# Kernel optimization log

Measured on AMD Instinct MI355X. Metric: run time of the kernel, lower is better.

## Reference

```python
import jax, jax.numpy as jnp
import numpy as np

# ---- fan-beam geometry config (uniform path: no pmatrix, uniform SID/SDD/angle/offcenter) ----
SID = 750.0          # source-to-isocenter distance (mm)
SDD = 1250.0         # source-to-detector distance (mm)
VIEWS = 128          # number of projection angles
NDET = 512           # detector element count
DET_ELT = 1.2        # detector element size (mm)
DET_OFF = 0.0        # detector offcenter (mm)
START_ANGLE = 0.0    # degrees
TOTAL_ANGLE = 360.0  # degrees
IMG_DIM = 256        # image is IMG_DIM x IMG_DIM
PIX = 1.0            # pixel size (mm)
STEP = 1.0           # fpjStepSize: ray sampling step (mm)
R = IMG_DIM * PIX * np.sqrt(2.0) / 2.0   # half image diagonal: ray segment to sample
NS = int(np.ceil(2.0 * R / STEP)) + 1    # samples per ray (static)


def _sample_points():
    # Per-view source / detector geometry; rays sampled from t = SID-R to SID+R.
    beta = jnp.asarray(np.deg2rad(START_ANGLE + TOTAL_ANGLE * np.arange(VIEWS) / VIEWS),
                       jnp.float32)                                    # [V]
    cb, sb = jnp.cos(beta), jnp.sin(beta)
    src = SID * jnp.stack([cb, sb], -1)                                 # [V,2] source position
    det0 = src - SDD * jnp.stack([cb, sb], -1)                          # [V,2] detector center
    eu = jnp.stack([-sb, cb], -1)                                       # [V,2] detector tangent
    u = (jnp.arange(NDET, dtype=jnp.float32) - (NDET - 1) / 2.0) * DET_ELT + DET_OFF  # [N]
    det = det0[:, None, :] + u[None, :, None] * eu[:, None, :]          # [V,N,2]
    d = det - src[:, None, :]
    d = d / jnp.linalg.norm(d, axis=-1, keepdims=True)                  # unit ray directions
    t = SID - R + STEP * jnp.arange(NS, dtype=jnp.float32)              # [NS]
    pts = src[:, None, None, :] + t[None, None, :, None] * d[:, :, None, :]  # [V,N,NS,2]
    return pts


def setup_inputs() -> dict:
    key = jax.random.key(0)
    x = jax.random.uniform(key, (2, IMG_DIM, IMG_DIM), dtype=jnp.float32)  # attenuation image batch
    return {"x": x}


def reference(x):
    # Ray-driven fan-beam forward projection: line integral via bilinear sampling.
    pts = _sample_points()                      # [V,N,NS,2] world coords (mm)
    px, py = pts[..., 0], pts[..., 1]
    jx = px / PIX + (IMG_DIM - 1) / 2.0         # continuous column index
    iy = (IMG_DIM - 1) / 2.0 - py / PIX         # continuous row index (y up)
    j0f = jnp.floor(jx)
    i0f = jnp.floor(iy)
    fj = jx - j0f
    fi = iy - i0f
    i0 = i0f.astype(jnp.int32)
    j0 = j0f.astype(jnp.int32)

    def gather(ii, jj):
        valid = (ii >= 0) & (ii < IMG_DIM) & (jj >= 0) & (jj < IMG_DIM)
        ic = jnp.clip(ii, 0, IMG_DIM - 1)
        jc = jnp.clip(jj, 0, IMG_DIM - 1)
        return x[:, ic, jc] * valid[None].astype(x.dtype)   # [B,V,N,NS]

    v00 = gather(i0, j0)
    v01 = gather(i0, j0 + 1)
    v10 = gather(i0 + 1, j0)
    v11 = gather(i0 + 1, j0 + 1)
    interp = (v00 * (1 - fi) * (1 - fj) + v01 * (1 - fi) * fj
              + v10 * fi * (1 - fj) + v11 * fi * fj)        # [B,V,N,NS]
    sinogram = interp.sum(-1) * STEP                        # [B,V,N]
    return sinogram
```

## Files before the change

### kernel.cpp

```cpp
#include <hip/hip_runtime.h>
#include <hip/hip_fp16.h>
#include <math.h>

constexpr int   VIEWS = 128;
constexpr int   NDET  = 512;
constexpr int   IMG   = 256;
constexpr int   BATCH = 2;
constexpr float SID_F = 750.0f;
constexpr float SDD_F = 1250.0f;
constexpr float DET_ELT = 1.2f;
constexpr float DET_OFF = 0.0f;
constexpr float STEP  = 1.0f;
constexpr int   NS = 364;
constexpr float T0 = (float)(750.0 - 181.01933598375618);

constexpr int PAD    = 2;
constexpr int TROWS  = IMG + 2 * PAD;
constexpr int TSTR   = 262;
constexpr int TWSTR  = TSTR / 2;
constexpr int TWORDS = TROWS * TWSTR;
constexpr int SPC    = NS / 2;

__global__ __launch_bounds__(1024) void fanbeam_lds(const float* __restrict__ img,
                                                    float* __restrict__ out) {
    __shared__ unsigned int tile32[TWORDS];
    __shared__ float red[1024];
    const int tid = threadIdx.x;
    const int blk = blockIdx.x;
    const int v = blk & (VIEWS - 1);
    const int b = blk >> 7;

    for (int k = tid; k < TWORDS; k += 1024) tile32[k] = 0u;
    __syncthreads();
    const float* __restrict__ src = img + b * IMG * IMG;
    for (int k = tid; k < (IMG * IMG) / 4; k += 1024) {
        const int p = k * 4;
        const int i = p >> 8;
        const int j = p & 255;
        const float4 f = *reinterpret_cast<const float4*>(src + p);
        const unsigned lo = ((unsigned)__half_as_ushort(__float2half(f.y)) << 16)
                          |  (unsigned)__half_as_ushort(__float2half(f.x));
        const unsigned hi = ((unsigned)__half_as_ushort(__float2half(f.w)) << 16)
                          |  (unsigned)__half_as_ushort(__float2half(f.z));
        const int h = (i + PAD) * TSTR + (j + PAD);
        tile32[h >> 1]       = lo;
        tile32[(h >> 1) + 1] = hi;
    }
    __syncthreads();

    const int n     = tid & (NDET - 1);
    const int chunk = tid >> 9;
    const float beta = (float)((double)v * 0.049087385212340517);
    const float cb = cosf(beta);
    const float sb = sinf(beta);
    const float u  = ((float)n - 255.5f) * DET_ELT + DET_OFF;
    float dx = fmaf(-u, sb, -SDD_F * cb);
    float dy = fmaf( u, cb, -SDD_F * sb);
    const float inv = rsqrtf(fmaf(dx, dx, dy * dy));
    dx *= inv;
    dy *= inv;
    const float cx = fmaf(SID_F, cb, 127.5f);
    const float cy = 127.5f - SID_F * sb;

    float acc = 0.0f;
    const int s0 = chunk * SPC;

#pragma unroll 4
    for (int s = 0; s < SPC; ++s) {
        const float t  = T0 + (float)(s0 + s);
        const float jx = fmaf(t, dx, cx);
        const float iy = fmaf(t, -dy, cy);
        const float j0f = floorf(jx);
        const float i0f = floorf(iy);
        const float fj = jx - j0f;
        const float fi = iy - i0f;
        int jp = (int)j0f + PAD;
        int ip = (int)i0f + PAD;
        jp = min(max(jp, 0), IMG + PAD);
        ip = min(max(ip, 0), IMG + PAD);
        const int w  = ip * TWSTR + (jp >> 1);
        const unsigned w0 = tile32[w];
        const unsigned w1 = tile32[w + 1];
        const unsigned w2 = tile32[w + TWSTR];
        const unsigned w3 = tile32[w + TWSTR + 1];
        const int sh = (jp & 1) << 4;
        const unsigned ptop = (unsigned)((((unsigned long long)w1 << 32) | w0) >> sh);
        const unsigned pbot = (unsigned)((((unsigned long long)w3 << 32) | w2) >> sh);
        const float2 ft = __half22float2(*reinterpret_cast<const __half2*>(&ptop));
        const float2 fb = __half22float2(*reinterpret_cast<const __half2*>(&pbot));
        const float top = fmaf(fj, ft.y - ft.x, ft.x);
        const float bot = fmaf(fj, fb.y - fb.x, fb.x);
        acc = fmaf(fi, bot - top, acc + top);
    }

    red[tid] = acc;
    __syncthreads();
    if (tid < 512) {
        out[blk * 512 + tid] = (red[tid] + red[tid + 512]) * STEP;
    }
}

extern "C" void kernel_launch(void* const* d_in, const int* in_sizes, int n_in,
                              void* d_out, int out_size, void* d_ws, size_t ws_size,
                              hipStream_t stream) {
    const float* x = (const float*)d_in[0];
    float* out = (float*)d_out;
    fanbeam_lds<<<BATCH * VIEWS, 1024, 0, stream>>>(x, out);
}
```

Baseline: 95.16 us.

## Clip ray sampling to image bounding box and zero only tile padding

Each ray's sample range is now clipped to the intersection of its line with the padded image square, so samples that fall entirely outside the image are skipped. The two thread halves interleave over even and odd samples instead of splitting into contiguous halves. Only the padding border of the LDS tile is zeroed, which removes the full clear and one barrier. The funnel shift becomes a single alignbit instruction and coordinates are clamped in float instead of int. Division by dx or dy can produce infinities for axis-aligned rays; the min/max logic is expected to handle that, but it adds edge-case risk.

```diff
diff --git a/kernel.cpp b/kernel.cpp
--- a/kernel.cpp
+++ b/kernel.cpp
@@ -19,7 +19,6 @@
 constexpr int TSTR   = 262;
 constexpr int TWSTR  = TSTR / 2;
 constexpr int TWORDS = TROWS * TWSTR;
-constexpr int SPC    = NS / 2;
 
 __global__ __launch_bounds__(1024) void fanbeam_lds(const float* __restrict__ img,
                                                     float* __restrict__ out) {
@@ -30,8 +29,21 @@
     const int v = blk & (VIEWS - 1);
     const int b = blk >> 7;
 
-    for (int k = tid; k < TWORDS; k += 1024) tile32[k] = 0u;
-    __syncthreads();
+    for (int k = tid; k < 524 + 768; k += 1024) {
+        int w;
+        if (k < 524) {
+            const int r = k / 131, c = k - r * 131;
+            const int row = (r < 2) ? r : 256 + r;
+            w = row * TWSTR + c;
+        } else {
+            const int kk = k - 524;
+            const int row = 2 + kk / 3;
+            const int m = kk % 3;
+            w = row * TWSTR + ((m == 0) ? 0 : 128 + m);
+        }
+        tile32[w] = 0u;
+    }
+
     const float* __restrict__ src = img + b * IMG * IMG;
     for (int k = tid; k < (IMG * IMG) / 4; k += 1024) {
         const int p = k * 4;
@@ -59,37 +71,55 @@
     const float inv = rsqrtf(fmaf(dx, dx, dy * dy));
     dx *= inv;
     dy *= inv;
-    const float cx = fmaf(SID_F, cb, 127.5f);
-    const float cy = 127.5f - SID_F * sb;
+    const float ndy = -dy;
+    const float sx = SID_F * cb;
+    const float sy = SID_F * sb;
+    const float cx = sx + 127.5f;
+    const float cy = 127.5f - sy;
+
+    const float invx = 1.0f / dx;
+    const float invy = 1.0f / dy;
+    const float ta = (-129.5f - sx) * invx, tb = (129.5f - sx) * invx;
+    const float tc = (-129.5f - sy) * invy, td = (129.5f - sy) * invy;
+    const float txmin = fminf(ta, tb), txmax = fmaxf(ta, tb);
+    const float tymin = fminf(tc, td), tymax = fmaxf(tc, td);
+    const float tmin = fmaxf(fmaxf(txmin, tymin), T0);
+    const float tmax = fminf(fminf(txmax, tymax), T0 + (float)(NS - 1));
+    int slo = (int)ceilf(tmin - T0);
+    int shi = (int)floorf(tmax - T0);
+    slo = max(slo, 0);
+    shi = min(shi, NS - 1);
 
     float acc = 0.0f;
-    const int s0 = chunk * SPC;
-
+    float sf = (float)(slo + chunk);
 #pragma unroll 4
-    for (int s = 0; s < SPC; ++s) {
-        const float t  = T0 + (float)(s0 + s);
-        const float jx = fmaf(t, dx, cx);
-        const float iy = fmaf(t, -dy, cy);
+    for (int s = slo + chunk; s <= shi; s += 2) {
+        const float t  = T0 + sf;
+        sf += 2.0f;
+        float jx = fmaf(t, dx, cx);
+        float iy = fmaf(t, ndy, cy);
+        jx = fminf(fmaxf(jx, -1.75f), 257.5f);
+        iy = fminf(fmaxf(iy, -1.75f), 256.5f);
         const float j0f = floorf(jx);
         const float i0f = floorf(iy);
         const float fj = jx - j0f;
         const float fi = iy - i0f;
-        int jp = (int)j0f + PAD;
-        int ip = (int)i0f + PAD;
-        jp = min(max(jp, 0), IMG + PAD);
-        ip = min(max(ip, 0), IMG + PAD);
+        const int jp = (int)j0f + PAD;
+        const int ip = (int)i0f + PAD;
         const int w  = ip * TWSTR + (jp >> 1);
         const unsigned w0 = tile32[w];
         const unsigned w1 = tile32[w + 1];
         const unsigned w2 = tile32[w + TWSTR];
         const unsigned w3 = tile32[w + TWSTR + 1];
-        const int sh = (jp & 1) << 4;
-        const unsigned ptop = (unsigned)((((unsigned long long)w1 << 32) | w0) >> sh);
-        const unsigned pbot = (unsigned)((((unsigned long long)w3 << 32) | w2) >> sh);
-        const float2 ft = __half22float2(*reinterpret_cast<const __half2*>(&ptop));
-        const float2 fb = __half22float2(*reinterpret_cast<const __half2*>(&pbot));
-        const float top = fmaf(fj, ft.y - ft.x, ft.x);
-        const float bot = fmaf(fj, fb.y - fb.x, fb.x);
+        const unsigned sh = (unsigned)(jp & 1) << 4;
+        const unsigned ptop = __builtin_amdgcn_alignbit(w1, w0, sh);
+        const unsigned pbot = __builtin_amdgcn_alignbit(w3, w2, sh);
+        const __half2 ht = *reinterpret_cast<const __half2*>(&ptop);
+        const __half2 hb = *reinterpret_cast<const __half2*>(&pbot);
+        const float t0v = __low2float(ht), t1v = __high2float(ht);
+        const float b0v = __low2float(hb), b1v = __high2float(hb);
+        const float top = fmaf(fj, t1v - t0v, t0v);
+        const float bot = fmaf(fj, b1v - b0v, b0v);
         acc = fmaf(fi, bot - top, acc + top);
     }
 
```

Measured after the change: 81.47 us. 14.4% less time.
